# Performance work log

Measured on AMD Instinct MI355X. Metric: run time of the kernel, lower is better.

The kernel has to match this reference:

```python
import jax, jax.numpy as jnp
import numpy as np


def rel_to_abs(x):
    """[b, hh, L, 2L-1] -> [b, hh, L, L] via pad/reshape trick."""
    b, hh, L, _ = x.shape
    x = jnp.pad(x, ((0, 0), (0, 0), (0, 0), (0, 1)))          # [b,hh,L,2L]
    flat = x.reshape(b, hh, L * 2 * L)
    flat = jnp.pad(flat, ((0, 0), (0, 0), (0, L - 1)))
    final = flat.reshape(b, hh, L + 1, 2 * L - 1)
    return final[:, :, :L, L - 1:]                             # [b,hh,L,L]


def relative_logits_1d(q, rel_k, transpose_mask):
    # q: [b, n, x, y, d]; rel_k: [2y-1, d]
    b, n, x, y, d = q.shape
    rel = jnp.einsum('bnxyd,md->bnxym', q, rel_k)
    rel = rel.reshape(b, n * x, y, 2 * y - 1)
    rel = rel_to_abs(rel)                                      # [b, n*x, y, y]
    rel = rel.reshape(b, n, x, y, y)
    rel = jnp.broadcast_to(rel[:, :, :, None, :, :], (b, n, x, x, y, y))
    return jnp.transpose(rel, transpose_mask)


def relative_logits(q, rel_emb_w, rel_emb_h):
    logits_w = relative_logits_1d(q, rel_emb_w, (0, 1, 2, 4, 3, 5))
    q_t = jnp.transpose(q, (0, 1, 3, 2, 4))  # swap h/w
    logits_h = relative_logits_1d(q_t, rel_emb_h, (0, 1, 4, 2, 5, 3))
    return logits_h + logits_w  # [b,n,h,w,h,w]


def setup_inputs() -> dict:
    key = jax.random.key(0)
    k1, k2, k3, k4, k5 = jax.random.split(key, 5)
    B, N, H, W, D = 4, 4, 48, 48, 32
    std = D ** (-0.5)
    return {
        'q': jax.random.normal(k1, (B, N, H, W, D), jnp.float32),
        'k': jax.random.normal(k2, (B, N, H, W, D), jnp.float32),
        'v': jax.random.normal(k3, (B, N, H, W, D), jnp.float32),
        'rel_emb_w': jax.random.normal(k4, (2 * W - 1, D), jnp.float32) * std,
        'rel_emb_h': jax.random.normal(k5, (2 * H - 1, D), jnp.float32) * std,
    }


def reference(q, k, v, rel_emb_w, rel_emb_h):
    bs, heads, h, w, dim = q.shape
    q = q * dim ** (-0.5)
    logits = jnp.einsum('bnhwd,bnpqd->bnhwpq', q, k)
    logits = logits + relative_logits(q, rel_emb_w, rel_emb_h)
    weights = jax.nn.softmax(logits.reshape(bs, heads, h, w, h * w), axis=-1)
    weights = weights.reshape(bs, heads, h, w, h, w)
    attn_out = jnp.einsum('bnhwpq,bnpqd->bhwnd', weights, v)
    # fold_heads=True
    return attn_out.reshape(bs, h, w, heads * dim)
```

## Files before the change

### kernel.cpp

```cpp
#include <hip/hip_runtime.h>
#include <hip/hip_bf16.h>


typedef __attribute__((ext_vector_type(8))) short bf16x8;
typedef __attribute__((ext_vector_type(4))) float f32x4;

#define DEVFN __device__ __forceinline__

#if __has_builtin(__builtin_amdgcn_exp2f)
#define EXP2(x) __builtin_amdgcn_exp2f(x)
#else
#define EXP2(x) exp2f(x)
#endif

constexpr int H_ = 48, W_ = 48, D_ = 32;
constexpr int L_ = H_ * W_;
constexpr int BN_ = 16;

constexpr int QB2 = 48;
constexpr int KB2 = 96;
constexpr int IT2 = L_ / KB2;
constexpr int QT2 = L_ / QB2;
constexpr int NWG2 = BN_ * QT2;

constexpr size_t WE_Q = 0;
constexpr size_t WE_K = 1179648;
constexpr size_t WE_V = 2359296;
constexpr size_t WE_R = 3538944;
constexpr size_t WS_NEED = (WE_R + 2 * 6 * 64 * 8) * 2;

DEVFN unsigned short f2bf(float f) {
  unsigned u = __float_as_uint(f);
  return (unsigned short)((u + 0x7fffu + ((u >> 16) & 1u)) >> 16);
}
DEVFN unsigned pk2(float lo, float hi) {
  return (unsigned)f2bf(lo) | ((unsigned)f2bf(hi) << 16);
}
DEVFN unsigned pkcvt(float lo, float hi) {
  __hip_bfloat162 h = __float22bfloat162_rn(make_float2(lo, hi));
  union { __hip_bfloat162 h2; unsigned u; } cv; cv.h2 = h;
  return cv.u;
}

template <int CTRL>
DEVFN float dppf(float x) {
  return __int_as_float(__builtin_amdgcn_update_dpp(0, __float_as_int(x), CTRL, 0xF, 0xF, true));
}
DEVFN float rowmax16(float x) {
  x = fmaxf(x, dppf<0x128>(x));
  x = fmaxf(x, dppf<0x124>(x));
  x = fmaxf(x, dppf<0x122>(x));
  x = fmaxf(x, dppf<0x121>(x));
  return x;
}
DEVFN float rowsum16(float x) {
  x += dppf<0x128>(x);
  x += dppf<0x124>(x);
  x += dppf<0x122>(x);
  x += dppf<0x121>(x);
  return x;
}

__global__ __launch_bounds__(256)
void prep_kernel(const float* __restrict__ Q, const float* __restrict__ K,
                 const float* __restrict__ V, const float* __restrict__ RW,
                 const float* __restrict__ RH, unsigned short* __restrict__ ws)
{
  __shared__ __align__(16) float Vl[3072];
  const int bid = blockIdx.x, tid = threadIdx.x;
  const float QS = 0.17677669529663687f * 1.4426950408889634f;
  if (bid < 576) {
    size_t e = ((size_t)bid * 256 + tid) * 8;
    const float* s = Q + e;
    float4 a = *(const float4*)s, c = *(const float4*)(s + 4);
    uint4 wv;
    wv.x = pkcvt(a.x * QS, a.y * QS); wv.y = pkcvt(a.z * QS, a.w * QS);
    wv.z = pkcvt(c.x * QS, c.y * QS); wv.w = pkcvt(c.z * QS, c.w * QS);
    *(uint4*)(ws + WE_Q + e) = wv;
  } else if (bid < 1152) {
    int idx = (bid - 576) * 256 + tid;
    int lane = idx & 63, t = idx >> 6;
    int l15 = lane & 15, lg = lane >> 4;
    int bn = t / 144, t16 = t % 144;
    int it = t16 / 6, kb = t16 % 6;
    int kbp = kb >> 1, f = kb & 1;
    int key96 = kbp * 32 + (l15 >> 2) * 8 + f * 4 + (l15 & 3);
    const float* s = K + ((size_t)(bn * L_ + it * 96 + key96) * D_ + lg * 8);
    float4 a = *(const float4*)s, c = *(const float4*)(s + 4);
    uint4 wv;
    wv.x = pkcvt(a.x, a.y); wv.y = pkcvt(a.z, a.w);
    wv.z = pkcvt(c.x, c.y); wv.w = pkcvt(c.z, c.w);
    *(uint4*)(ws + WE_K + (size_t)idx * 8) = wv;
  } else if (bid < 1536) {
    const int tile = bid - 1152;
    const float* src = V + (size_t)tile * 96 * D_;
    #pragma unroll
    for (int u = 0; u < 3; ++u)
      ((float4*)Vl)[tid + u * 256] = ((const float4*)src)[tid + u * 256];
    __syncthreads();
    unsigned short* dst = ws + WE_V + (size_t)tile * 3072;
    #pragma unroll
    for (int u = 0; u < 2; ++u) {
      const int f2i = tid + u * 256;
      if (f2i < 384) {
        const int f2 = f2i >> 6, lane = f2i & 63;
        const int l15 = lane & 15, lg = lane >> 4;
        const int kbp = f2 >> 1, half = f2 & 1;
        const int d = half * 16 + l15;
        float fv[8];
        #pragma unroll
        for (int j = 0; j < 8; ++j)
          fv[j] = Vl[(kbp * 32 + lg * 8 + j) * 32 + d];
        uint4 wv;
        wv.x = pkcvt(fv[0], fv[1]); wv.y = pkcvt(fv[2], fv[3]);
        wv.z = pkcvt(fv[4], fv[5]); wv.w = pkcvt(fv[6], fv[7]);
        *(uint4*)(dst + (size_t)f2i * 8) = wv;
      }
    }
  } else {
    int t = (bid - 1536) * 256 + tid;
    if (t < 768) {
      int tbl = t / 384, rem = t % 384, jb = rem / 64, lane = rem % 64;
      int l15 = lane & 15, lg = lane >> 4;
      int j = jb * 16 + l15;
      int jc = (j > 94) ? 94 : j;
      const float* s = (tbl ? RW : RH) + jc * D_ + lg * 8;
      float4 a = *(const float4*)s, c = *(const float4*)(s + 4);
      uint4 wv;
      wv.x = pkcvt(a.x, a.y); wv.y = pkcvt(a.z, a.w);
      wv.z = pkcvt(c.x, c.y); wv.w = pkcvt(c.z, c.w);
      *(uint4*)(ws + WE_R + (size_t)t * 8) = wv;
    }
  }
}

__global__ __launch_bounds__(192, 2)
void relattn4(const unsigned short* __restrict__ ws, float* __restrict__ OUT)
{
  __shared__ __align__(16) float BhT[48 * 50];
  __shared__ __align__(16) float BwT[48 * 52];

  const unsigned short* Qb = ws + WE_Q;
  const unsigned short* Kf = ws + WE_K;
  const unsigned short* Vf = ws + WE_V;
  const unsigned short* Rf = ws + WE_R;

  const int bid = blockIdx.x;
  const int wg  = (bid & 7) * (NWG2 / 8) + (bid >> 3);
  const int bn  = wg / QT2;
  const int qb  = (wg % QT2) * QB2;
  const int b   = bn >> 2, n = bn & 3;

  const int tid  = threadIdx.x;
  const int wave = tid >> 6;
  const int lane = tid & 63;
  const int l15  = lane & 15;
  const int lg   = lane >> 4;

  const int qi = qb + wave * 16 + l15;
  const bf16x8 qfrag = *(const bf16x8*)(Qb + (size_t)(bn * L_ + qi) * D_ + lg * 8);

  const f32x4 z4 = {0.f, 0.f, 0.f, 0.f};

  int hq[4], wq[4];
  #pragma unroll
  for (int r = 0; r < 4; ++r) {
    int qg = qb + wave * 16 + lg * 4 + r;
    hq[r] = qg / 48; wq[r] = qg % 48;
  }

  #pragma unroll
  for (int jb = 0; jb < 6; ++jb) {
    bf16x8 rhf = *(const bf16x8*)(Rf + ((0 * 6 + jb) * 64 + lane) * 8);
    bf16x8 rwf = *(const bf16x8*)(Rf + ((1 * 6 + jb) * 64 + lane) * 8);
    f32x4 mh = __builtin_amdgcn_mfma_f32_16x16x32_bf16(qfrag, rhf, z4, 0, 0, 0);
    f32x4 mw = __builtin_amdgcn_mfma_f32_16x16x32_bf16(qfrag, rwf, z4, 0, 0, 0);
    const int j = jb * 16 + l15;
    if (j < 95) {
      #pragma unroll
      for (int r = 0; r < 4; ++r) {
        const int row = wave * 16 + lg * 4 + r;
        const int p  = j - 47 + hq[r];
        if (p >= 0 && p < 48)  BhT[row * 50 + p]  = mh[r];
        const int ww = j - 47 + wq[r];
        if (ww >= 0 && ww < 48) BwT[row * 52 + ww] = mw[r];
      }
    }
  }

  const int q52 = (wave * 16 + l15) * 52;
  const int bt0 = lg * 8;
  const int bt1 = (lg < 2) ? (lg * 8 + 32) : (lg * 8 - 16);
  const int bt2 = lg * 8 + 16;
  float bwv[3][8];
  *(float4*)&bwv[0][0] = *(const float4*)&BwT[q52 + bt0];
  *(float4*)&bwv[0][4] = *(const float4*)&BwT[q52 + bt0 + 4];
  *(float4*)&bwv[1][0] = *(const float4*)&BwT[q52 + bt1];
  *(float4*)&bwv[1][4] = *(const float4*)&BwT[q52 + bt1 + 4];
  *(float4*)&bwv[2][0] = *(const float4*)&BwT[q52 + bt2];
  *(float4*)&bwv[2][4] = *(const float4*)&BwT[q52 + bt2 + 4];

  const unsigned short* KfB = Kf + (size_t)bn * 24 * 3072 + (size_t)lane * 8;
  const unsigned short* VfB = Vf + (size_t)bn * 24 * 3072 + (size_t)lane * 8;

  f32x4 acc0 = z4, acc1 = z4;
  float l_acc = 0.f;

  const float* bhrow = &BhT[(wave * 16 + l15) * 50];
  const bool lglo = (lg < 2);

  for (int it = 0; it < IT2; ++it) {
    const unsigned short* kt = KfB + (size_t)it * 3072;
    const unsigned short* vt = VfB + (size_t)it * 3072;
    bf16x8 kf[6], vf[6];
    #pragma unroll
    for (int u = 0; u < 6; ++u) kf[u] = *(const bf16x8*)(kt + u * 512);
    #pragma unroll
    for (int u = 0; u < 6; ++u) vf[u] = *(const bf16x8*)(vt + u * 512);

    const float2 bh2 = *(const float2*)(bhrow + it * 2);
    const float bhm = lglo ? bh2.x : bh2.y;

    #pragma unroll
    for (int kbp = 0; kbp < 3; ++kbp) {
      const float bhsel = (kbp == 0) ? bh2.x : ((kbp == 2) ? bh2.y : bhm);
      f32x4 cin0, cin1;
      #pragma unroll
      for (int r = 0; r < 4; ++r) {
        cin0[r] = bhsel + bwv[kbp][r];
        cin1[r] = bhsel + bwv[kbp][4 + r];
      }
      f32x4 s0 = __builtin_amdgcn_mfma_f32_16x16x32_bf16(kf[kbp * 2 + 0], qfrag, cin0, 0, 0, 0);
      f32x4 s1 = __builtin_amdgcn_mfma_f32_16x16x32_bf16(kf[kbp * 2 + 1], qfrag, cin1, 0, 0, 0);

      const float e0 = EXP2(s0[0]), e1 = EXP2(s0[1]), e2 = EXP2(s0[2]), e3 = EXP2(s0[3]);
      const float e4 = EXP2(s1[0]), e5 = EXP2(s1[1]), e6 = EXP2(s1[2]), e7 = EXP2(s1[3]);
      l_acc += (((e0 + e1) + (e2 + e3)) + ((e4 + e5) + (e6 + e7)));
      union { unsigned u[4]; bf16x8 v; } pf;
      pf.u[0] = pkcvt(e0, e1); pf.u[1] = pkcvt(e2, e3);
      pf.u[2] = pkcvt(e4, e5); pf.u[3] = pkcvt(e6, e7);

      acc0 = __builtin_amdgcn_mfma_f32_16x16x32_bf16(vf[kbp * 2 + 0], pf.v, acc0, 0, 0, 0);
      acc1 = __builtin_amdgcn_mfma_f32_16x16x32_bf16(vf[kbp * 2 + 1], pf.v, acc1, 0, 0, 0);
    }
  }

  float ls = l_acc;
  ls += __shfl_xor(ls, 16);
  ls += __shfl_xor(ls, 32);
  const float inv = __builtin_amdgcn_rcpf(ls);
  const int ql = qb + wave * 16 + l15;
  const int hql = ql / 48, wql = ql % 48;
  float* op = OUT + ((size_t)(b * 48 + hql) * 48 + wql) * 128 + n * 32 + lg * 4;
  *(float4*)op        = make_float4(acc0[0] * inv, acc0[1] * inv, acc0[2] * inv, acc0[3] * inv);
  *(float4*)(op + 16) = make_float4(acc1[0] * inv, acc1[1] * inv, acc1[2] * inv, acc1[3] * inv);
}

__global__ __launch_bounds__(256, 2)
void relattn_kernel(const float* __restrict__ Q, const float* __restrict__ K,
                    const float* __restrict__ V, const float* __restrict__ RW,
                    const float* __restrict__ RH, float* __restrict__ OUT)
{
  __shared__ __align__(16) unsigned short Klds[64][40];
  __shared__ __align__(16) unsigned       VT[32][36];
  __shared__ __align__(16) unsigned short Plds[4][16][72];
  __shared__ __align__(16) float          Bh[64][49];
  __shared__ __align__(16) float          Bw[64][49];

  const int bid = blockIdx.x;
  const int wg  = (bid & 7) * 72 + (bid >> 3);
  const int bn  = wg / 36;
  const int qb  = (wg % 36) * 64;
  const int b   = bn >> 2, n = bn & 3;

  const int tid  = threadIdx.x;
  const int wave = tid >> 6;
  const int lane = tid & 63;
  const int l15  = lane & 15;
  const int lg   = lane >> 4;

  const float QS = 0.17677669529663687f * 1.4426950408889634f;
  const int qi = qb + wave * 16 + l15;
  bf16x8 qfrag;
  {
    const float* qr = Q + ((bn * L_ + qi) * D_ + lg * 8);
    float4 a = *(const float4*)qr;
    float4 c = *(const float4*)(qr + 4);
    qfrag[0] = (short)f2bf(a.x * QS); qfrag[1] = (short)f2bf(a.y * QS);
    qfrag[2] = (short)f2bf(a.z * QS); qfrag[3] = (short)f2bf(a.w * QS);
    qfrag[4] = (short)f2bf(c.x * QS); qfrag[5] = (short)f2bf(c.y * QS);
    qfrag[6] = (short)f2bf(c.z * QS); qfrag[7] = (short)f2bf(c.w * QS);
  }
  const f32x4 z4 = {0.f, 0.f, 0.f, 0.f};
  #pragma unroll
  for (int jb = 0; jb < 6; ++jb) {
    const int j  = jb * 16 + l15;
    const int jc = (j > 94) ? 94 : j;
    bf16x8 rhf, rwf;
    {
      const float* rr = RH + jc * D_ + lg * 8;
      float4 a = *(const float4*)rr; float4 c = *(const float4*)(rr + 4);
      rhf[0] = (short)f2bf(a.x); rhf[1] = (short)f2bf(a.y);
      rhf[2] = (short)f2bf(a.z); rhf[3] = (short)f2bf(a.w);
      rhf[4] = (short)f2bf(c.x); rhf[5] = (short)f2bf(c.y);
      rhf[6] = (short)f2bf(c.z); rhf[7] = (short)f2bf(c.w);
      const float* rr2 = RW + jc * D_ + lg * 8;
      float4 a2 = *(const float4*)rr2; float4 c2 = *(const float4*)(rr2 + 4);
      rwf[0] = (short)f2bf(a2.x); rwf[1] = (short)f2bf(a2.y);
      rwf[2] = (short)f2bf(a2.z); rwf[3] = (short)f2bf(a2.w);
      rwf[4] = (short)f2bf(c2.x); rwf[5] = (short)f2bf(c2.y);
      rwf[6] = (short)f2bf(c2.z); rwf[7] = (short)f2bf(c2.w);
    }
    f32x4 mh = __builtin_amdgcn_mfma_f32_16x16x32_bf16(qfrag, rhf, z4, 0, 0, 0);
    f32x4 mw = __builtin_amdgcn_mfma_f32_16x16x32_bf16(qfrag, rwf, z4, 0, 0, 0);
    #pragma unroll
    for (int r = 0; r < 4; ++r) {
      const int qrow = lg * 4 + r;
      const int qg   = qb + wave * 16 + qrow;
      const int hqv  = qg / 48, wqv = qg % 48;
      if (j < 95) {
        const int p  = j - 47 + hqv;
        if (p >= 0 && p < 48) Bh[wave * 16 + qrow][p] = mh[r];
        const int ww = j - 47 + wqv;
        if (ww >= 0 && ww < 48) Bw[wave * 16 + qrow][ww] = mw[r];
      }
    }
  }
  float bw0[4], bw1[4], bw2[4];
  #pragma unroll
  for (int r = 0; r < 4; ++r) {
    bw0[r] = Bw[wave * 16 + lg * 4 + r][ 0 + l15];
    bw1[r] = Bw[wave * 16 + lg * 4 + r][16 + l15];
    bw2[r] = Bw[wave * 16 + lg * 4 + r][32 + l15];
  }
  f32x4 acc0 = z4, acc1 = z4;
  float m_r[4] = {-INFINITY, -INFINITY, -INFINITY, -INFINITY};
  float l_r[4] = {0.f, 0.f, 0.f, 0.f};
  const float* kbase = K + bn * L_ * D_;
  const float* vbase = V + bn * L_ * D_;
  for (int it = 0; it < 36; ++it) {
    const int kv0 = it * 64;
    __syncthreads();
    {
      const int r = tid >> 2, c = (tid & 3) * 8;
      const float* s = kbase + (kv0 + r) * D_ + c;
      float4 a = *(const float4*)s; float4 cc = *(const float4*)(s + 4);
      uint4 wv;
      wv.x = pk2(a.x, a.y);  wv.y = pk2(a.z, a.w);
      wv.z = pk2(cc.x, cc.y); wv.w = pk2(cc.z, cc.w);
      *(uint4*)&Klds[r][c] = wv;
    }
    {
      const int kp = tid >> 3, dg = tid & 7;
      const float* s0 = vbase + (kv0 + 2 * kp) * D_ + dg * 4;
      float4 a = *(const float4*)s0;
      float4 c = *(const float4*)(s0 + D_);
      VT[dg * 4 + 0][kp] = pk2(a.x, c.x);
      VT[dg * 4 + 1][kp] = pk2(a.y, c.y);
      VT[dg * 4 + 2][kp] = pk2(a.z, c.z);
      VT[dg * 4 + 3][kp] = pk2(a.w, c.w);
    }
    __syncthreads();
    f32x4 sacc[4];
    #pragma unroll
    for (int kb = 0; kb < 4; ++kb) {
      bf16x8 kf = *(const bf16x8*)&Klds[kb * 16 + l15][lg * 8];
      sacc[kb] = __builtin_amdgcn_mfma_f32_16x16x32_bf16(qfrag, kf, z4, 0, 0, 0);
    }
    const int p0   = kv0 / 48;
    const int tthr = (p0 + 1) * 48 - kv0;
    const int m0   = it % 3;
    float bh0[4], bh1[4];
    #pragma unroll
    for (int r = 0; r < 4; ++r) {
      bh0[r] = Bh[wave * 16 + lg * 4 + r][p0];
      bh1[r] = Bh[wave * 16 + lg * 4 + r][p0 + 1];
    }
    #pragma unroll
    for (int kb = 0; kb < 4; ++kb) {
      const bool hi = (kb * 16 + l15) >= tthr;
      int mm = m0 + kb; if (mm >= 3) mm -= 3; if (mm >= 3) mm -= 3;
      #pragma unroll
      for (int r = 0; r < 4; ++r) {
        const float bwv2 = (mm == 0) ? bw0[r] : ((mm == 1) ? bw1[r] : bw2[r]);
        sacc[kb][r] += (hi ? bh1[r] : bh0[r]) + bwv2;
      }
    }
    #pragma unroll
    for (int r = 0; r < 4; ++r) {
      float mx = fmaxf(fmaxf(sacc[0][r], sacc[1][r]), fmaxf(sacc[2][r], sacc[3][r]));
      mx = rowmax16(mx);
      const float mn = fmaxf(m_r[r], mx);
      const float sc = exp2f(m_r[r] - mn);
      m_r[r] = mn;
      acc0[r] *= sc; acc1[r] *= sc;
      const float pe0 = exp2f(sacc[0][r] - mn);
      const float pe1 = exp2f(sacc[1][r] - mn);
      const float pe2 = exp2f(sacc[2][r] - mn);
      const float pe3 = exp2f(sacc[3][r] - mn);
      const float rs = rowsum16(pe0 + pe1 + pe2 + pe3);
      l_r[r] = l_r[r] * sc + rs;
      const int prow = lg * 4 + r;
      Plds[wave][prow][ 0 + l15] = f2bf(pe0);
      Plds[wave][prow][16 + l15] = f2bf(pe1);
      Plds[wave][prow][32 + l15] = f2bf(pe2);
      Plds[wave][prow][48 + l15] = f2bf(pe3);
    }
    const unsigned short* VTu = (const unsigned short*)VT;
    #pragma unroll
    for (int s2 = 0; s2 < 2; ++s2) {
      bf16x8 a2 = *(const bf16x8*)&Plds[wave][l15][s2 * 32 + lg * 8];
      bf16x8 b0 = *(const bf16x8*)&VTu[( 0 + l15) * 72 + s2 * 32 + lg * 8];
      bf16x8 b1 = *(const bf16x8*)&VTu[(16 + l15) * 72 + s2 * 32 + lg * 8];
      acc0 = __builtin_amdgcn_mfma_f32_16x16x32_bf16(a2, b0, acc0, 0, 0, 0);
      acc1 = __builtin_amdgcn_mfma_f32_16x16x32_bf16(a2, b1, acc1, 0, 0, 0);
    }
  }
  #pragma unroll
  for (int r = 0; r < 4; ++r) {
    const int qg = qb + wave * 16 + lg * 4 + r;
    const int hqv = qg / 48, wqv = qg % 48;
    const float inv = __builtin_amdgcn_rcpf(l_r[r]);
    float* op = OUT + ((b * 48 + hqv) * 48 + wqv) * 128 + n * 32 + l15;
    op[0]  = acc0[r] * inv;
    op[16] = acc1[r] * inv;
  }
}

extern "C" void kernel_launch(void* const* d_in, const int* in_sizes, int n_in,
                              void* d_out, int out_size, void* d_ws, size_t ws_size,
                              hipStream_t stream) {
  const float* q  = (const float*)d_in[0];
  const float* k  = (const float*)d_in[1];
  const float* v  = (const float*)d_in[2];
  const float* rw = (const float*)d_in[3];
  const float* rh = (const float*)d_in[4];
  float* out = (float*)d_out;
  if (ws_size >= WS_NEED) {
    unsigned short* ws = (unsigned short*)d_ws;
    hipLaunchKernelGGL(prep_kernel, dim3(1539), dim3(256), 0, stream, q, k, v, rw, rh, ws);
    hipLaunchKernelGGL(relattn4, dim3(NWG2), dim3(192), 0, stream, ws, out);
  } else {
    hipLaunchKernelGGL(relattn_kernel, dim3(576), dim3(256), 0, stream, q, k, v, rw, rh, out);
  }
}
```

Baseline: 50.60 us.

## Double-buffer K/V register prefetch, factor height bias out of exp, raise occupancy

The main loop is restructured so each K/V tile is loaded into a second register set while the previous tile is computed, with sched_barrier fences holding that order. The height bias is no longer added into the MFMA accumulator input; exp2 of it is computed once per iteration and multiplied onto the exponentials. Width-bias values are re-read from LDS each iteration instead of kept in registers, and launch bounds go from 2 to 3 blocks per CU to allow more resident waves. The prefetch runs one tile past the end on the last iteration, so it reads unused workspace memory. The extra per-element multiply and the per-iteration LDS reads cost some issue slots.

```diff
diff --git a/kernel.cpp b/kernel.cpp
--- a/kernel.cpp
+++ b/kernel.cpp
@@ -134,8 +134,8 @@
   }
 }
 
-__global__ __launch_bounds__(192, 2)
-void relattn4(const unsigned short* __restrict__ ws, float* __restrict__ OUT)
+__global__ __launch_bounds__(192, 3)
+void relattn6(const unsigned short* __restrict__ ws, float* __restrict__ OUT)
 {
   __shared__ __align__(16) float BhT[48 * 50];
   __shared__ __align__(16) float BwT[48 * 52];
@@ -161,13 +161,6 @@
   const bf16x8 qfrag = *(const bf16x8*)(Qb + (size_t)(bn * L_ + qi) * D_ + lg * 8);
 
   const f32x4 z4 = {0.f, 0.f, 0.f, 0.f};
-
-  int hq[4], wq[4];
-  #pragma unroll
-  for (int r = 0; r < 4; ++r) {
-    int qg = qb + wave * 16 + lg * 4 + r;
-    hq[r] = qg / 48; wq[r] = qg % 48;
-  }
 
   #pragma unroll
   for (int jb = 0; jb < 6; ++jb) {
@@ -179,26 +172,20 @@
     if (j < 95) {
       #pragma unroll
       for (int r = 0; r < 4; ++r) {
+        const int qg = qb + wave * 16 + lg * 4 + r;
         const int row = wave * 16 + lg * 4 + r;
-        const int p  = j - 47 + hq[r];
+        const int p  = j - 47 + qg / 48;
         if (p >= 0 && p < 48)  BhT[row * 50 + p]  = mh[r];
-        const int ww = j - 47 + wq[r];
+        const int ww = j - 47 + qg % 48;
         if (ww >= 0 && ww < 48) BwT[row * 52 + ww] = mw[r];
       }
     }
   }
 
   const int q52 = (wave * 16 + l15) * 52;
-  const int bt0 = lg * 8;
-  const int bt1 = (lg < 2) ? (lg * 8 + 32) : (lg * 8 - 16);
-  const int bt2 = lg * 8 + 16;
-  float bwv[3][8];
-  *(float4*)&bwv[0][0] = *(const float4*)&BwT[q52 + bt0];
-  *(float4*)&bwv[0][4] = *(const float4*)&BwT[q52 + bt0 + 4];
-  *(float4*)&bwv[1][0] = *(const float4*)&BwT[q52 + bt1];
-  *(float4*)&bwv[1][4] = *(const float4*)&BwT[q52 + bt1 + 4];
-  *(float4*)&bwv[2][0] = *(const float4*)&BwT[q52 + bt2];
-  *(float4*)&bwv[2][4] = *(const float4*)&BwT[q52 + bt2 + 4];
+  const float* bwp0 = &BwT[q52 + lg * 8];
+  const float* bwp1 = &BwT[q52 + ((lg < 2) ? (lg * 8 + 32) : (lg * 8 - 16))];
+  const float* bwp2 = &BwT[q52 + lg * 8 + 16];
 
   const unsigned short* KfB = Kf + (size_t)bn * 24 * 3072 + (size_t)lane * 8;
   const unsigned short* VfB = Vf + (size_t)bn * 24 * 3072 + (size_t)lane * 8;
@@ -209,41 +196,55 @@
   const float* bhrow = &BhT[(wave * 16 + l15) * 50];
   const bool lglo = (lg < 2);
 
-  for (int it = 0; it < IT2; ++it) {
-    const unsigned short* kt = KfB + (size_t)it * 3072;
-    const unsigned short* vt = VfB + (size_t)it * 3072;
-    bf16x8 kf[6], vf[6];
-    #pragma unroll
-    for (int u = 0; u < 6; ++u) kf[u] = *(const bf16x8*)(kt + u * 512);
-    #pragma unroll
-    for (int u = 0; u < 6; ++u) vf[u] = *(const bf16x8*)(vt + u * 512);
-
-    const float2 bh2 = *(const float2*)(bhrow + it * 2);
-    const float bhm = lglo ? bh2.x : bh2.y;
-
-    #pragma unroll
-    for (int kbp = 0; kbp < 3; ++kbp) {
-      const float bhsel = (kbp == 0) ? bh2.x : ((kbp == 2) ? bh2.y : bhm);
-      f32x4 cin0, cin1;
-      #pragma unroll
-      for (int r = 0; r < 4; ++r) {
-        cin0[r] = bhsel + bwv[kbp][r];
-        cin1[r] = bhsel + bwv[kbp][4 + r];
-      }
-      f32x4 s0 = __builtin_amdgcn_mfma_f32_16x16x32_bf16(kf[kbp * 2 + 0], qfrag, cin0, 0, 0, 0);
-      f32x4 s1 = __builtin_amdgcn_mfma_f32_16x16x32_bf16(kf[kbp * 2 + 1], qfrag, cin1, 0, 0, 0);
-
-      const float e0 = EXP2(s0[0]), e1 = EXP2(s0[1]), e2 = EXP2(s0[2]), e3 = EXP2(s0[3]);
-      const float e4 = EXP2(s1[0]), e5 = EXP2(s1[1]), e6 = EXP2(s1[2]), e7 = EXP2(s1[3]);
-      l_acc += (((e0 + e1) + (e2 + e3)) + ((e4 + e5) + (e6 + e7)));
-      union { unsigned u[4]; bf16x8 v; } pf;
-      pf.u[0] = pkcvt(e0, e1); pf.u[1] = pkcvt(e2, e3);
-      pf.u[2] = pkcvt(e4, e5); pf.u[3] = pkcvt(e6, e7);
-
-      acc0 = __builtin_amdgcn_mfma_f32_16x16x32_bf16(vf[kbp * 2 + 0], pf.v, acc0, 0, 0, 0);
-      acc1 = __builtin_amdgcn_mfma_f32_16x16x32_bf16(vf[kbp * 2 + 1], pf.v, acc1, 0, 0, 0);
-    }
-  }
+  bf16x8 kfA[6], vfA[6], kfB[6], vfB[6];
+
+#define LOADIT(kfX, vfX, itv) do {                                          \
+    const unsigned short* kt_ = KfB + (size_t)(itv) * 3072;                 \
+    const unsigned short* vt_ = VfB + (size_t)(itv) * 3072;                 \
+    _Pragma("unroll") for (int u = 0; u < 6; ++u)                           \
+      kfX[u] = *(const bf16x8*)(kt_ + u * 512);                             \
+    _Pragma("unroll") for (int u = 0; u < 6; ++u)                           \
+      vfX[u] = *(const bf16x8*)(vt_ + u * 512);                             \
+  } while (0)
+
+#define COMPUTE(itv, kfX, vfX) do {                                         \
+    const float2 bh2_ = *(const float2*)(bhrow + (itv) * 2);                \
+    const float bhf0_ = EXP2(bh2_.x), bhf1_ = EXP2(bh2_.y);                 \
+    const float bhfm_ = lglo ? bhf0_ : bhf1_;                               \
+    _Pragma("unroll") for (int kbp = 0; kbp < 3; ++kbp) {                   \
+      const float* bwp_ = (kbp == 0) ? bwp0 : ((kbp == 1) ? bwp1 : bwp2);   \
+      f32x4 cin0 = *(const f32x4*)(bwp_);                                   \
+      f32x4 cin1 = *(const f32x4*)(bwp_ + 4);                               \
+      f32x4 s0 = __builtin_amdgcn_mfma_f32_16x16x32_bf16(kfX[kbp*2+0], qfrag, cin0, 0, 0, 0); \
+      f32x4 s1 = __builtin_amdgcn_mfma_f32_16x16x32_bf16(kfX[kbp*2+1], qfrag, cin1, 0, 0, 0); \
+      const float bf_ = (kbp == 0) ? bhf0_ : ((kbp == 2) ? bhf1_ : bhfm_);  \
+      const float e0 = EXP2(s0[0]) * bf_, e1 = EXP2(s0[1]) * bf_;           \
+      const float e2 = EXP2(s0[2]) * bf_, e3 = EXP2(s0[3]) * bf_;           \
+      const float e4 = EXP2(s1[0]) * bf_, e5 = EXP2(s1[1]) * bf_;           \
+      const float e6 = EXP2(s1[2]) * bf_, e7 = EXP2(s1[3]) * bf_;           \
+      l_acc += (((e0 + e1) + (e2 + e3)) + ((e4 + e5) + (e6 + e7)));         \
+      union { unsigned u[4]; bf16x8 v; } pf_;                               \
+      pf_.u[0] = pkcvt(e0, e1); pf_.u[1] = pkcvt(e2, e3);                   \
+      pf_.u[2] = pkcvt(e4, e5); pf_.u[3] = pkcvt(e6, e7);                   \
+      acc0 = __builtin_amdgcn_mfma_f32_16x16x32_bf16(vfX[kbp*2+0], pf_.v, acc0, 0, 0, 0); \
+      acc1 = __builtin_amdgcn_mfma_f32_16x16x32_bf16(vfX[kbp*2+1], pf_.v, acc1, 0, 0, 0); \
+    }                                                                       \
+  } while (0)
+
+  LOADIT(kfA, vfA, 0);
+  for (int it2 = 0; it2 < IT2 / 2; ++it2) {
+    const int itA = it2 * 2;
+    __builtin_amdgcn_sched_barrier(0);
+    LOADIT(kfB, vfB, itA + 1);
+    __builtin_amdgcn_sched_barrier(0);
+    COMPUTE(itA, kfA, vfA);
+    __builtin_amdgcn_sched_barrier(0);
+    LOADIT(kfA, vfA, itA + 2);
+    __builtin_amdgcn_sched_barrier(0);
+    COMPUTE(itA + 1, kfB, vfB);
+  }
+#undef LOADIT
+#undef COMPUTE
 
   float ls = l_acc;
   ls += __shfl_xor(ls, 16);
@@ -439,7 +440,7 @@
   if (ws_size >= WS_NEED) {
     unsigned short* ws = (unsigned short*)d_ws;
     hipLaunchKernelGGL(prep_kernel, dim3(1539), dim3(256), 0, stream, q, k, v, rw, rh, ws);
-    hipLaunchKernelGGL(relattn4, dim3(NWG2), dim3(192), 0, stream, ws, out);
+    hipLaunchKernelGGL(relattn6, dim3(NWG2), dim3(192), 0, stream, ws, out);
   } else {
     hipLaunchKernelGGL(relattn_kernel, dim3(576), dim3(256), 0, stream, q, k, v, rw, rh, out);
   }
```

After: 42.53 us. -16.0%, faster.
